# Performance work log

Hardware: AMD Instinct MI355X
Metric: run time of the kernel (lower is better)

Reference implementation:

```python
import math
import jax, jax.numpy as jnp
import numpy as np

B, S, D, H = 2, 2048, 1024, 16
DH = D // H


def setup_inputs() -> dict:
    key = jax.random.key(0)
    ks = jax.random.split(key, 12)
    s = 1.0 / math.sqrt(D)
    return {
        "x_q": jax.random.normal(ks[0], (B, S, D), jnp.float32),
        "x_k": jax.random.normal(ks[1], (B, S, D), jnp.float32),
        "x_v": jax.random.normal(ks[2], (B, S, D), jnp.float32),
        "mask": jax.random.randint(ks[3], (B, S), 0, 2) > 0,
        "Wq": jax.random.normal(ks[4], (D, D), jnp.float32) * s,
        "bq": jnp.zeros((D,), jnp.float32),
        "Wk": jax.random.normal(ks[5], (D, D), jnp.float32) * s,
        "bk": jnp.zeros((D,), jnp.float32),
        "Wv": jax.random.normal(ks[6], (D, D), jnp.float32) * s,
        "bv": jnp.zeros((D,), jnp.float32),
        "Wo": jax.random.normal(ks[7], (D, D), jnp.float32) * s,
        "bo": jnp.zeros((D,), jnp.float32),
    }


def reference(x_q, x_k, x_v, mask, Wq, bq, Wk, bk, Wv, bv, Wo, bo):
    # nn.Linear: y = x @ W^T + b
    Q = jnp.einsum('bsd,ed->bse', x_q, Wq) + bq
    K = jnp.einsum('bsd,ed->bse', x_k, Wk) + bk
    V = jnp.einsum('bsd,ed->bse', x_v, Wv) + bv
    b, sq, d = Q.shape
    # split(dim_split, 2) + cat(dim=0) == per-head attention on [B,S,H,DH]
    Qh = Q.reshape(b, sq, H, DH)
    Kh = K.reshape(b, -1, H, DH)
    Vh = V.reshape(b, -1, H, DH)
    scores = jnp.einsum('bqhd,bkhd->bhqk', Qh, Kh) / math.sqrt(DH)
    # inf_mask: -1e9 where mask is False, broadcast over heads and queries
    scores = scores + jnp.where(mask[:, None, None, :], 0.0, -1e9)
    A = jax.nn.softmax(scores, axis=-1)  # dropout is identity in eval
    out = jnp.einsum('bhqk,bkhd->bqhd', A, Vh).reshape(b, sq, d)
    return jnp.einsum('bsd,ed->bse', out, Wo) + bo
```

## Files before the change

### kernel.cpp

```cpp
#include <hip/hip_runtime.h>
#include <hip/hip_bf16.h>
#include <stdint.h>

#define BB  2
#define SS  2048
#define DDIM 1024
#define HH  16
#define DH  64

typedef __attribute__((ext_vector_type(8))) short short8;
typedef __attribute__((ext_vector_type(4))) short short4v;
typedef __attribute__((ext_vector_type(4))) float float4v;

#define AS1 __attribute__((address_space(1)))
#define AS3 __attribute__((address_space(3)))

static __device__ __forceinline__ void gl2lds16(const void* g, void* l) {
  __builtin_amdgcn_global_load_lds((const AS1 unsigned int*)g,
                                   (AS3 unsigned int*)l, 16, 0, 0);
}

static __device__ __forceinline__ float bf2f(short s) {
  union { unsigned u; float f; } c;
  c.u = ((unsigned)(unsigned short)s) << 16;
  return c.f;
}
static __device__ __forceinline__ short f2bf(float f) {
  union { float ff; unsigned u; } c;
  c.ff = f;
  unsigned u = c.u;
  u += 0x7fffu + ((u >> 16) & 1u);
  return (short)(u >> 16);
}

#if __has_builtin(__builtin_amdgcn_exp2f)
static __device__ __forceinline__ float exp2fast(float x) { return __builtin_amdgcn_exp2f(x); }
#else
static __device__ __forceinline__ float exp2fast(float x) { return __expf(x * 0.69314718056f); }
#endif

static __device__ __forceinline__ unsigned packbf(float x, float y) {
  unsigned ax = __float_as_uint(x) + 0x8000u;
  unsigned ay = __float_as_uint(y) + 0x8000u;
#if __has_builtin(__builtin_amdgcn_perm)
  return __builtin_amdgcn_perm(ay, ax, 0x07060302u);
#else
  return (ax >> 16) | (ay & 0xffff0000u);
#endif
}

static __device__ __forceinline__ int detect_f32(const void* p) {
  const float* f = (const float*)p;
  int ok = 1;
#pragma unroll
  for (int i = 0; i < 16; i++) {
    float a = fabsf(f[i]);
    ok &= (a > 1e-10f && a < 1e4f) ? 1 : 0;
  }
  return ok;
}

struct CvtArgs {
  const void* xq; const void* xk; const void* xv;
  const void* wq; const void* wk; const void* wv; const void* wo;
  const void* b0; const void* b1; const void* b2; const void* b3;
  const int* mask;
  short* dst;
  float* mw;
};

__global__ __launch_bounds__(256)
void cvt_kernel(CvtArgs a) {
  const int f32m = detect_f32(a.xq);
  const size_t gtid = (size_t)blockIdx.x * blockDim.x + threadIdx.x;
  const size_t stride = (size_t)gridDim.x * blockDim.x;
  const size_t M4 = (size_t)4 << 20, M1 = (size_t)1 << 20, TOT = (size_t)16 << 20;
  for (size_t i = gtid; i * 4 < TOT; i += stride) {
    const size_t idx = i * 4;
    const void* src;
    size_t off;
    if (idx < 3 * M4) {
      size_t xi = idx / M4;
      off = idx & (M4 - 1);
      src = (xi == 0) ? a.xq : (xi == 1) ? a.xk : a.xv;
    } else {
      size_t wi = (idx - 3 * M4) / M1;
      off = idx & (M1 - 1);
      src = (wi == 0) ? a.wq : (wi == 1) ? a.wk : (wi == 2) ? a.wv : a.wo;
    }
    short4v o;
    if (f32m) {
      float4v v = *(const float4v*)((const float*)src + off);
#pragma unroll
      for (int j = 0; j < 4; j++) o[j] = f2bf(v[j]);
    } else {
      o = *(const short4v*)((const short*)src + off);
    }
    *(short4v*)(a.dst + idx) = o;
  }
  if (gtid < 1024) {
    const void* bs[4] = {a.b0, a.b1, a.b2, a.b3};
#pragma unroll
    for (int j = 0; j < 4; j++) {
      short v = f32m ? f2bf(((const float*)bs[j])[gtid])
                     : ((const short*)bs[j])[gtid];
      a.dst[TOT + (size_t)j * 1024 + gtid] = v;
    }
  }
  if (gtid < BB * SS)
    a.mw[gtid] = a.mask[gtid] ? -23.083120654223414f : -1e9f;
}

struct GemmArgs {
  const short* x[3];
  const short* w[3];
  const short* b[3];
  short* o[3];
  const void* probe;
  int tmask;
  int detect_out;
};

__global__ __launch_bounds__(256)
void gemm_kernel(GemmArgs a) {
  constexpr int GK = 1024, GN = 1024;
  __shared__ alignas(16) short As[128 * 32];
  __shared__ alignas(16) short Bs[128 * 32];

  const int t = threadIdx.x;
  const int w = t >> 6, l = t & 63, l15 = l & 15, qd = l >> 4;
  const int bn = blockIdx.x, bm = blockIdx.y, mat = blockIdx.z;

  const short* X  = a.x[mat];
  const short* W  = a.w[mat];
  const short* Bi = a.b[mat];
  short* O        = a.o[mat];
  const int transposed = (a.tmask >> mat) & 1;

  const short* Ag = X + (size_t)bm * 128 * GK;
  const short* Bg = W + (size_t)bn * 128 * GK;

  const int L0 = t, L1 = 256 + t;
  const int r0 = L0 >> 2, g0 = (L0 & 3) ^ ((r0 >> 1) & 3);
  const int r1 = L1 >> 2, g1 = (L1 & 3) ^ ((r1 >> 1) & 3);
  const size_t off0 = (size_t)r0 * GK + g0 * 8;
  const size_t off1 = (size_t)r1 * GK + g1 * 8;

  float4v acc[4][4];
#pragma unroll
  for (int i = 0; i < 4; i++)
#pragma unroll
    for (int j = 0; j < 4; j++) acc[i][j] = (float4v){0.f, 0.f, 0.f, 0.f};

  const int wm = (w >> 1) * 64, wn = (w & 1) * 64;

  for (int k0 = 0; k0 < GK; k0 += 32) {
    gl2lds16(Ag + off0 + k0, (char*)As + L0 * 16);
    gl2lds16(Ag + off1 + k0, (char*)As + L1 * 16);
    gl2lds16(Bg + off0 + k0, (char*)Bs + L0 * 16);
    gl2lds16(Bg + off1 + k0, (char*)Bs + L1 * 16);
    __syncthreads();

    short8 af[4], bf[4];
#pragma unroll
    for (int i = 0; i < 4; i++) {
      int m = wm + i * 16 + l15;
      af[i] = *(const short8*)((const char*)As + (m * 4 + (qd ^ ((m >> 1) & 3))) * 16);
      int n = wn + i * 16 + l15;
      bf[i] = *(const short8*)((const char*)Bs + (n * 4 + (qd ^ ((n >> 1) & 3))) * 16);
    }
#pragma unroll
    for (int i = 0; i < 4; i++)
#pragma unroll
      for (int j = 0; j < 4; j++)
        acc[i][j] = __builtin_amdgcn_mfma_f32_16x16x32_bf16(af[i], bf[j], acc[i][j], 0, 0, 0);
    __syncthreads();
  }

  if (!transposed) {
    const int outf32 = a.detect_out ? detect_f32(a.probe) : 0;
    float bj[4];
#pragma unroll
    for (int j = 0; j < 4; j++) bj[j] = bf2f(Bi[bn * 128 + wn + j * 16 + l15]);
#pragma unroll
    for (int i = 0; i < 4; i++) {
      int mgl = bm * 128 + wm + i * 16 + qd * 4;
#pragma unroll
      for (int j = 0; j < 4; j++) {
        int ngl = bn * 128 + wn + j * 16 + l15;
        if (outf32) {
          float* Of = (float*)O;
#pragma unroll
          for (int r = 0; r < 4; r++)
            Of[(size_t)(mgl + r) * GN + ngl] = acc[i][j][r] + bj[j];
        } else {
#pragma unroll
          for (int r = 0; r < 4; r++)
            O[(size_t)(mgl + r) * GN + ngl] = f2bf(acc[i][j][r] + bj[j]);
        }
      }
    }
  } else {
#pragma unroll
    for (int j = 0; j < 4; j++) {
      int ngl = bn * 128 + wn + j * 16 + l15;
      float bb = bf2f(Bi[ngl]);
#pragma unroll
      for (int i = 0; i < 4; i++) {
        int mgl = bm * 128 + wm + i * 16 + qd * 4;
        int bidx = mgl >> 11;
        int s = mgl & (SS - 1);
        short4v v;
#pragma unroll
        for (int r = 0; r < 4; r++) v[r] = f2bf(acc[i][j][r] + bb);
        *(short4v*)(O + (size_t)bidx * DDIM * SS + (size_t)ngl * SS + s) = v;
      }
    }
  }
}

__global__ __launch_bounds__(128)
void flash_kernel(const short* __restrict__ Q, const short* __restrict__ K,
                  const short* __restrict__ Vt, const float* __restrict__ Mw,
                  short* __restrict__ At) {
  __shared__ alignas(16) short Kbuf[2][2][2048];
  __shared__ alignas(16) short Vbuf[2][2][2048];

  const int t = threadIdx.x;
  const int w = t >> 6, l = t & 63, l15 = l & 15, qd = l >> 4;
  const int bh = blockIdx.x, qt = blockIdx.y;
  const int b = bh >> 4, h = bh & 15;
  const int q0 = qt * 64 + w * 32;

  const float SC = 0.125f * 1.44269504f;

  short8 qf[2][2];
#pragma unroll
  for (int g = 0; g < 2; g++) {
    const short* Qb = Q + ((size_t)(b * SS + q0 + 16 * g + l15)) * DDIM + h * 64;
#pragma unroll
    for (int c = 0; c < 2; c++) qf[g][c] = *(const short8*)(Qb + 32 * c + 8 * qd);
  }

  const short ov = (l15 == 0) ? (short)0x3F80 : (short)0;
  const short8 onesf = {ov, ov, ov, ov, ov, ov, ov, ov};

  const short* Kg = K + ((size_t)(b * SS + (l >> 3))) * DDIM + h * 64
                    + ((l & 7) ^ ((l >> 3) & 7)) * 8;
  const short* Vg = Vt + (size_t)b * DDIM * SS + (size_t)(h * 64 + (l >> 2)) * SS
                    + ((l & 3) ^ ((l >> 3) & 3)) * 8;
  const float* MwB = Mw + b * SS;

  char* Kw = (char*)Kbuf[w];
  char* Vw = (char*)Vbuf[w];

  float4v oacc[2][4], oaccl[2];
#pragma unroll
  for (int g = 0; g < 2; g++) {
    oaccl[g] = (float4v){0.f, 0.f, 0.f, 0.f};
#pragma unroll
    for (int mt = 0; mt < 4; mt++) oacc[g][mt] = (float4v){0.f, 0.f, 0.f, 0.f};
  }

  const int sv2 = 2 * ((l15 >> 1) & 3);
  const int kswz = l15 & 7;

  float4v maC[2], maN[2];

  {
#pragma unroll
    for (int j = 0; j < 4; j++)
      gl2lds16(Kg + (size_t)(j * 8) * DDIM, Kw + j * 1024 + (l << 4));
#pragma unroll
    for (int j = 0; j < 4; j++)
      gl2lds16(Vg + (size_t)(j * 16) * SS, Vw + j * 1024 + (l << 4));
#pragma unroll
    for (int mt = 0; mt < 2; mt++)
      maC[mt] = *(const float4v*)(MwB + mt * 16 + 4 * qd);
  }

  auto body = [&](int i, int bb) {
    asm volatile("s_waitcnt vmcnt(0)" ::: "memory");

    if (i < 63) {
      const int nb = bb ^ 1;
      const size_t koff = (size_t)((i + 1) * 32) * DDIM;
#pragma unroll
      for (int j = 0; j < 4; j++)
        gl2lds16(Kg + koff + (size_t)(j * 8) * DDIM, Kw + nb * 4096 + j * 1024 + (l << 4));
      const int voff = (i + 1) * 32;
#pragma unroll
      for (int j = 0; j < 4; j++)
        gl2lds16(Vg + voff + (size_t)(j * 16) * SS, Vw + nb * 4096 + j * 1024 + (l << 4));
#pragma unroll
      for (int mt = 0; mt < 2; mt++)
        maN[mt] = *(const float4v*)(MwB + (i + 1) * 32 + mt * 16 + 4 * qd);
    }

    const short* ksb = (const short*)(Kw + bb * 4096);
    const short* vsb = (const short*)(Vw + bb * 4096);

    float4v sacc[2][2];
#pragma unroll
    for (int g = 0; g < 2; g++)
#pragma unroll
      for (int mt = 0; mt < 2; mt++) sacc[g][mt] = (float4v){0.f, 0.f, 0.f, 0.f};
#pragma unroll
    for (int c = 0; c < 2; c++) {
#pragma unroll
      for (int mt = 0; mt < 2; mt++) {
        short8 kf = *(const short8*)(ksb + (mt * 16 + l15) * 64 + (((c * 4 + qd) ^ kswz) * 8));
#pragma unroll
        for (int g = 0; g < 2; g++)
          sacc[g][mt] = __builtin_amdgcn_mfma_f32_16x16x32_bf16(kf, qf[g][c], sacc[g][mt], 0, 0, 0);
      }
    }

    union { short4v h[2]; short8 v8; } vf[4];
#pragma unroll
    for (int mt = 0; mt < 4; mt++) {
      const short* vr = vsb + (mt * 16 + l15) * 32;
      vf[mt].h[0] = *(const short4v*)(vr + ((qd ^ sv2) * 4));
      vf[mt].h[1] = *(const short4v*)(vr + (((4 + qd) ^ sv2) * 4));
    }

#pragma unroll
    for (int g = 0; g < 2; g++) {
      float p0[4], p1[4];
#pragma unroll
      for (int r = 0; r < 4; r++) {
        p0[r] = exp2fast(fmaf(sacc[g][0][r], SC, maC[0][r]));
        p1[r] = exp2fast(fmaf(sacc[g][1][r], SC, maC[1][r]));
      }
      union { unsigned u[4]; short8 v8; } pk;
      pk.u[0] = packbf(p0[0], p0[1]);
      pk.u[1] = packbf(p0[2], p0[3]);
      pk.u[2] = packbf(p1[0], p1[1]);
      pk.u[3] = packbf(p1[2], p1[3]);

#pragma unroll
      for (int mt = 0; mt < 4; mt++)
        oacc[g][mt] = __builtin_amdgcn_mfma_f32_16x16x32_bf16(vf[mt].v8, pk.v8, oacc[g][mt], 0, 0, 0);
      oaccl[g] = __builtin_amdgcn_mfma_f32_16x16x32_bf16(onesf, pk.v8, oaccl[g], 0, 0, 0);
    }

    maC[0] = maN[0];
    maC[1] = maN[1];
  };

  for (int i = 0; i < 64; i += 2) {
    body(i, 0);
    body(i + 1, 1);
  }

#pragma unroll
  for (int g = 0; g < 2; g++) {
    const float lg = __shfl(oaccl[g][0], l15);
    const float inv = 1.f / lg;
    short* Og = At + ((size_t)(b * SS + q0 + 16 * g + l15)) * DDIM + h * 64;
#pragma unroll
    for (int mt = 0; mt < 4; mt++) {
      short4v v;
#pragma unroll
      for (int r = 0; r < 4; r++) v[r] = f2bf(oacc[g][mt][r] * inv);
      *(short4v*)(Og + mt * 16 + qd * 4) = v;
    }
  }
}

extern "C" void kernel_launch(void* const* d_in, const int* in_sizes, int n_in,
                              void* d_out, int out_size, void* d_ws, size_t ws_size,
                              hipStream_t stream) {
  (void)in_sizes; (void)n_in; (void)out_size; (void)ws_size;
  const int* mask = (const int*)d_in[3];

  char* ws = (char*)d_ws;
  short* wsBF = (short*)ws;
  const size_t M1 = (size_t)1 << 20;
  short* Qb = (short*)(ws + (size_t)34 * M1);
  short* Kb = (short*)(ws + (size_t)42 * M1);
  short* Vt = (short*)(ws + (size_t)50 * M1);
  short* At = (short*)(ws + (size_t)58 * M1);
  float* Mw = (float*)(ws + (size_t)66 * M1);

  CvtArgs c;
  c.xq = d_in[0]; c.xk = d_in[1]; c.xv = d_in[2];
  c.wq = d_in[4]; c.wk = d_in[6]; c.wv = d_in[8]; c.wo = d_in[10];
  c.b0 = d_in[5]; c.b1 = d_in[7]; c.b2 = d_in[9]; c.b3 = d_in[11];
  c.mask = mask; c.dst = wsBF; c.mw = Mw;
  hipLaunchKernelGGL(cvt_kernel, dim3(4096), dim3(256), 0, stream, c);

  GemmArgs a1;
  a1.x[0] = wsBF;            a1.x[1] = wsBF + 4 * M1;  a1.x[2] = wsBF + 8 * M1;
  a1.w[0] = wsBF + 12 * M1;  a1.w[1] = wsBF + 13 * M1; a1.w[2] = wsBF + 14 * M1;
  a1.b[0] = wsBF + 16 * M1;  a1.b[1] = wsBF + 16 * M1 + 1024;
  a1.b[2] = wsBF + 16 * M1 + 2048;
  a1.o[0] = Qb; a1.o[1] = Kb; a1.o[2] = Vt;
  a1.probe = d_in[0];
  a1.tmask = 4;
  a1.detect_out = 0;
  hipLaunchKernelGGL(gemm_kernel, dim3(8, 32, 3), dim3(256), 0, stream, a1);

  hipLaunchKernelGGL(flash_kernel, dim3(32, 32), dim3(128), 0, stream,
                     Qb, Kb, Vt, Mw, At);

  GemmArgs a2;
  a2.x[0] = At;             a2.w[0] = wsBF + 15 * M1;
  a2.b[0] = wsBF + 16 * M1 + 3072;
  a2.o[0] = (short*)d_out;
  a2.x[1] = a2.x[2] = At; a2.w[1] = a2.w[2] = a2.w[0];
  a2.b[1] = a2.b[2] = a2.b[0]; a2.o[1] = a2.o[2] = a2.o[0];
  a2.probe = d_in[0];
  a2.tmask = 0;
  a2.detect_out = 1;
  hipLaunchKernelGGL(gemm_kernel, dim3(8, 32, 1), dim3(256), 0, stream, a2);
}
```

Measured before the change: 263.4 us.

## Load K/V tiles directly into registers and use single-wave flash blocks

The flash attention kernel drops the LDS staging of K and V tiles. Each lane now loads its MFMA operand fragments straight from global memory into double-buffered register sets, and the software pipeline alternates between A and B tiles. The launch becomes one 64-thread wave per block, with batch-head as the fastest-varying index so that blocks sharing K/V run together and hit in L2. This removes the LDS round trip and the waitcnt stalls, at the cost of less coalesced global loads and higher register pressure.

Result: slower. 375.7 us (+42.6%).

```diff
diff --git a/kernel.cpp b/kernel.cpp
--- a/kernel.cpp
+++ b/kernel.cpp
@@ -219,18 +219,15 @@
   }
 }
 
-__global__ __launch_bounds__(128)
+__global__ __launch_bounds__(64)
 void flash_kernel(const short* __restrict__ Q, const short* __restrict__ K,
                   const short* __restrict__ Vt, const float* __restrict__ Mw,
                   short* __restrict__ At) {
-  __shared__ alignas(16) short Kbuf[2][2][2048];
-  __shared__ alignas(16) short Vbuf[2][2][2048];
-
-  const int t = threadIdx.x;
-  const int w = t >> 6, l = t & 63, l15 = l & 15, qd = l >> 4;
-  const int bh = blockIdx.x, qt = blockIdx.y;
+  const int l = threadIdx.x, l15 = l & 15, qd = l >> 4;
+  const int x = blockIdx.x;
+  const int bh = x & 31, qt = x >> 5;
   const int b = bh >> 4, h = bh & 15;
-  const int q0 = qt * 64 + w * 32;
+  const int q0 = qt * 32;
 
   const float SC = 0.125f * 1.44269504f;
 
@@ -245,14 +242,20 @@
   const short ov = (l15 == 0) ? (short)0x3F80 : (short)0;
   const short8 onesf = {ov, ov, ov, ov, ov, ov, ov, ov};
 
-  const short* Kg = K + ((size_t)(b * SS + (l >> 3))) * DDIM + h * 64
-                    + ((l & 7) ^ ((l >> 3) & 7)) * 8;
-  const short* Vg = Vt + (size_t)b * DDIM * SS + (size_t)(h * 64 + (l >> 2)) * SS
-                    + ((l & 3) ^ ((l >> 3) & 3)) * 8;
-  const float* MwB = Mw + b * SS;
-
-  char* Kw = (char*)Kbuf[w];
-  char* Vw = (char*)Vbuf[w];
+  const short* kp[2];
+#pragma unroll
+  for (int mt = 0; mt < 2; mt++)
+    kp[mt] = K + ((size_t)(b * SS + 16 * mt + l15)) * DDIM + h * 64 + 8 * qd;
+  const short* vp[4];
+#pragma unroll
+  for (int mt = 0; mt < 4; mt++)
+    vp[mt] = Vt + (size_t)b * DDIM * SS + (size_t)(h * 64 + 16 * mt + l15) * SS + 4 * qd;
+  const float* mp = Mw + b * SS + 4 * qd;
+
+  short8 kfA[2][2], kfB[2][2];
+  union VF { short4v h[2]; short8 v8; };
+  VF vfA[4], vfB[4];
+  float4v maA[2], maB[2];
 
   float4v oacc[2][4], oaccl[2];
 #pragma unroll
@@ -262,96 +265,63 @@
     for (int mt = 0; mt < 4; mt++) oacc[g][mt] = (float4v){0.f, 0.f, 0.f, 0.f};
   }
 
-  const int sv2 = 2 * ((l15 >> 1) & 3);
-  const int kswz = l15 & 7;
-
-  float4v maC[2], maN[2];
-
-  {
-#pragma unroll
-    for (int j = 0; j < 4; j++)
-      gl2lds16(Kg + (size_t)(j * 8) * DDIM, Kw + j * 1024 + (l << 4));
-#pragma unroll
-    for (int j = 0; j < 4; j++)
-      gl2lds16(Vg + (size_t)(j * 16) * SS, Vw + j * 1024 + (l << 4));
-#pragma unroll
-    for (int mt = 0; mt < 2; mt++)
-      maC[mt] = *(const float4v*)(MwB + mt * 16 + 4 * qd);
-  }
-
-  auto body = [&](int i, int bb) {
-    asm volatile("s_waitcnt vmcnt(0)" ::: "memory");
-
-    if (i < 63) {
-      const int nb = bb ^ 1;
-      const size_t koff = (size_t)((i + 1) * 32) * DDIM;
-#pragma unroll
-      for (int j = 0; j < 4; j++)
-        gl2lds16(Kg + koff + (size_t)(j * 8) * DDIM, Kw + nb * 4096 + j * 1024 + (l << 4));
-      const int voff = (i + 1) * 32;
-#pragma unroll
-      for (int j = 0; j < 4; j++)
-        gl2lds16(Vg + voff + (size_t)(j * 16) * SS, Vw + nb * 4096 + j * 1024 + (l << 4));
+#define LOAD_TILE(KF, VF_, MA, i)                                              \
+  do {                                                                         \
+    const size_t krow = (size_t)(i) * 32 * DDIM;                               \
+    _Pragma("unroll") for (int mt = 0; mt < 2; mt++) {                         \
+      KF[mt][0] = *(const short8*)(kp[mt] + krow);                             \
+      KF[mt][1] = *(const short8*)(kp[mt] + krow + 32);                        \
+    }                                                                          \
+    _Pragma("unroll") for (int mt = 0; mt < 4; mt++) {                         \
+      VF_[mt].h[0] = *(const short4v*)(vp[mt] + (i) * 32);                     \
+      VF_[mt].h[1] = *(const short4v*)(vp[mt] + (i) * 32 + 16);                \
+    }                                                                          \
+    _Pragma("unroll") for (int mt = 0; mt < 2; mt++)                           \
+      MA[mt] = *(const float4v*)(mp + (i) * 32 + 16 * mt);                     \
+  } while (0)
+
+  auto compute = [&](short8 kf[2][2], VF vf[4], float4v ma[2]) {
+    float4v sacc[2][2];
+#pragma unroll
+    for (int g = 0; g < 2; g++)
+#pragma unroll
+      for (int mt = 0; mt < 2; mt++) sacc[g][mt] = (float4v){0.f, 0.f, 0.f, 0.f};
+#pragma unroll
+    for (int c = 0; c < 2; c++)
 #pragma unroll
       for (int mt = 0; mt < 2; mt++)
-        maN[mt] = *(const float4v*)(MwB + (i + 1) * 32 + mt * 16 + 4 * qd);
-    }
-
-    const short* ksb = (const short*)(Kw + bb * 4096);
-    const short* vsb = (const short*)(Vw + bb * 4096);
-
-    float4v sacc[2][2];
-#pragma unroll
-    for (int g = 0; g < 2; g++)
-#pragma unroll
-      for (int mt = 0; mt < 2; mt++) sacc[g][mt] = (float4v){0.f, 0.f, 0.f, 0.f};
-#pragma unroll
-    for (int c = 0; c < 2; c++) {
-#pragma unroll
-      for (int mt = 0; mt < 2; mt++) {
-        short8 kf = *(const short8*)(ksb + (mt * 16 + l15) * 64 + (((c * 4 + qd) ^ kswz) * 8));
 #pragma unroll
         for (int g = 0; g < 2; g++)
-          sacc[g][mt] = __builtin_amdgcn_mfma_f32_16x16x32_bf16(kf, qf[g][c], sacc[g][mt], 0, 0, 0);
-      }
-    }
-
-    union { short4v h[2]; short8 v8; } vf[4];
-#pragma unroll
-    for (int mt = 0; mt < 4; mt++) {
-      const short* vr = vsb + (mt * 16 + l15) * 32;
-      vf[mt].h[0] = *(const short4v*)(vr + ((qd ^ sv2) * 4));
-      vf[mt].h[1] = *(const short4v*)(vr + (((4 + qd) ^ sv2) * 4));
-    }
+          sacc[g][mt] = __builtin_amdgcn_mfma_f32_16x16x32_bf16(kf[mt][c], qf[g][c], sacc[g][mt], 0, 0, 0);
 
 #pragma unroll
     for (int g = 0; g < 2; g++) {
       float p0[4], p1[4];
 #pragma unroll
       for (int r = 0; r < 4; r++) {
-        p0[r] = exp2fast(fmaf(sacc[g][0][r], SC, maC[0][r]));
-        p1[r] = exp2fast(fmaf(sacc[g][1][r], SC, maC[1][r]));
+        p0[r] = exp2fast(fmaf(sacc[g][0][r], SC, ma[0][r]));
+        p1[r] = exp2fast(fmaf(sacc[g][1][r], SC, ma[1][r]));
       }
       union { unsigned u[4]; short8 v8; } pk;
       pk.u[0] = packbf(p0[0], p0[1]);
       pk.u[1] = packbf(p0[2], p0[3]);
       pk.u[2] = packbf(p1[0], p1[1]);
       pk.u[3] = packbf(p1[2], p1[3]);
-
 #pragma unroll
       for (int mt = 0; mt < 4; mt++)
         oacc[g][mt] = __builtin_amdgcn_mfma_f32_16x16x32_bf16(vf[mt].v8, pk.v8, oacc[g][mt], 0, 0, 0);
       oaccl[g] = __builtin_amdgcn_mfma_f32_16x16x32_bf16(onesf, pk.v8, oaccl[g], 0, 0, 0);
     }
-
-    maC[0] = maN[0];
-    maC[1] = maN[1];
   };
 
+  LOAD_TILE(kfA, vfA, maA, 0);
   for (int i = 0; i < 64; i += 2) {
-    body(i, 0);
-    body(i + 1, 1);
-  }
+    if (i + 1 < 64) LOAD_TILE(kfB, vfB, maB, i + 1);
+    compute(kfA, vfA, maA);
+    if (i + 2 < 64) LOAD_TILE(kfA, vfA, maA, i + 2);
+    compute(kfB, vfB, maB);
+  }
+#undef LOAD_TILE
 
 #pragma unroll
   for (int g = 0; g < 2; g++) {
@@ -401,7 +371,7 @@
   a1.detect_out = 0;
   hipLaunchKernelGGL(gemm_kernel, dim3(8, 32, 3), dim3(256), 0, stream, a1);
 
-  hipLaunchKernelGGL(flash_kernel, dim3(32, 32), dim3(128), 0, stream,
+  hipLaunchKernelGGL(flash_kernel, dim3(64 * 32), dim3(64), 0, stream,
                      Qb, Kb, Vt, Mw, At);
 
   GemmArgs a2;
```

## Share K/V tiles across four waves in flash attention with block barriers

Applied to the files above, without the earlier changes.

The flash kernel moves from 2-wave blocks, where each wave loads its own 32-key K/V slices, to 4-wave blocks covering 128 queries. The four waves now share double-buffered 64-key K and V tiles in LDS, loaded cooperatively, plus a small mask-add buffer. This cuts redundant global-to-LDS traffic per query and halves the iteration count. In exchange it adds a block-wide barrier every iteration, halves the grid size, and changes the LDS swizzle for V.

New measurement: 245.9 us. 6.6% less time.

```diff
diff --git a/kernel.cpp b/kernel.cpp
--- a/kernel.cpp
+++ b/kernel.cpp
@@ -219,18 +219,19 @@
   }
 }
 
-__global__ __launch_bounds__(128)
+__global__ __launch_bounds__(256)
 void flash_kernel(const short* __restrict__ Q, const short* __restrict__ K,
                   const short* __restrict__ Vt, const float* __restrict__ Mw,
                   short* __restrict__ At) {
-  __shared__ alignas(16) short Kbuf[2][2][2048];
-  __shared__ alignas(16) short Vbuf[2][2][2048];
+  __shared__ alignas(16) short Ks[2][64 * 64];
+  __shared__ alignas(16) short Vs[2][64 * 64];
+  __shared__ alignas(16) float madd[2][64];
 
   const int t = threadIdx.x;
   const int w = t >> 6, l = t & 63, l15 = l & 15, qd = l >> 4;
   const int bh = blockIdx.x, qt = blockIdx.y;
   const int b = bh >> 4, h = bh & 15;
-  const int q0 = qt * 64 + w * 32;
+  const int q0 = qt * 128 + w * 32;
 
   const float SC = 0.125f * 1.44269504f;
 
@@ -245,14 +246,13 @@
   const short ov = (l15 == 0) ? (short)0x3F80 : (short)0;
   const short8 onesf = {ov, ov, ov, ov, ov, ov, ov, ov};
 
-  const short* Kg = K + ((size_t)(b * SS + (l >> 3))) * DDIM + h * 64
-                    + ((l & 7) ^ ((l >> 3) & 7)) * 8;
-  const short* Vg = Vt + (size_t)b * DDIM * SS + (size_t)(h * 64 + (l >> 2)) * SS
-                    + ((l & 3) ^ ((l >> 3) & 3)) * 8;
+  const int kr = t >> 3;
+  const short* Kg = K + ((size_t)(b * SS + kr)) * DDIM + h * 64
+                    + ((t & 7) ^ (kr & 7)) * 8;
+  const int vr = t >> 3;
+  const short* Vg = Vt + (size_t)b * DDIM * SS + (size_t)(h * 64 + vr) * SS
+                    + ((t & 7) ^ (vr & 7)) * 8;
   const float* MwB = Mw + b * SS;
-
-  char* Kw = (char*)Kbuf[w];
-  char* Vw = (char*)Vbuf[w];
 
   float4v oacc[2][4], oaccl[2];
 #pragma unroll
@@ -262,95 +262,90 @@
     for (int mt = 0; mt < 4; mt++) oacc[g][mt] = (float4v){0.f, 0.f, 0.f, 0.f};
   }
 
-  const int sv2 = 2 * ((l15 >> 1) & 3);
-  const int kswz = l15 & 7;
-
-  float4v maC[2], maN[2];
-
-  {
-#pragma unroll
-    for (int j = 0; j < 4; j++)
-      gl2lds16(Kg + (size_t)(j * 8) * DDIM, Kw + j * 1024 + (l << 4));
-#pragma unroll
-    for (int j = 0; j < 4; j++)
-      gl2lds16(Vg + (size_t)(j * 16) * SS, Vw + j * 1024 + (l << 4));
-#pragma unroll
-    for (int mt = 0; mt < 2; mt++)
-      maC[mt] = *(const float4v*)(MwB + mt * 16 + 4 * qd);
-  }
-
-  auto body = [&](int i, int bb) {
-    asm volatile("s_waitcnt vmcnt(0)" ::: "memory");
-
-    if (i < 63) {
-      const int nb = bb ^ 1;
-      const size_t koff = (size_t)((i + 1) * 32) * DDIM;
-#pragma unroll
-      for (int j = 0; j < 4; j++)
-        gl2lds16(Kg + koff + (size_t)(j * 8) * DDIM, Kw + nb * 4096 + j * 1024 + (l << 4));
-      const int voff = (i + 1) * 32;
-#pragma unroll
-      for (int j = 0; j < 4; j++)
-        gl2lds16(Vg + voff + (size_t)(j * 16) * SS, Vw + nb * 4096 + j * 1024 + (l << 4));
-#pragma unroll
-      for (int mt = 0; mt < 2; mt++)
-        maN[mt] = *(const float4v*)(MwB + (i + 1) * 32 + mt * 16 + 4 * qd);
-    }
-
-    const short* ksb = (const short*)(Kw + bb * 4096);
-    const short* vsb = (const short*)(Vw + bb * 4096);
-
-    float4v sacc[2][2];
+  const int swz = l15 & 7;
+
+  gl2lds16(Kg, (char*)Ks[0] + t * 16);
+  gl2lds16(Kg + (size_t)32 * DDIM, (char*)Ks[0] + 4096 + t * 16);
+  gl2lds16(Vg, (char*)Vs[0] + t * 16);
+  gl2lds16(Vg + 32 * SS, (char*)Vs[0] + 4096 + t * 16);
+  float mwN = 0.f;
+  if (t < 64) {
+    madd[0][t] = MwB[t];
+    mwN = MwB[64 + t];
+  }
+
+  for (int i = 0; i < 32; i++) {
+    const int cur = i & 1, nxt = cur ^ 1;
+    asm volatile("s_waitcnt vmcnt(0) lgkmcnt(0)\n\ts_barrier" ::: "memory");
+
+    if (i < 31) {
+      const size_t ko = (size_t)((i + 1) * 64) * DDIM;
+      gl2lds16(Kg + ko, (char*)Ks[nxt] + t * 16);
+      gl2lds16(Kg + ko + (size_t)32 * DDIM, (char*)Ks[nxt] + 4096 + t * 16);
+      const int vo = (i + 1) * 64;
+      gl2lds16(Vg + vo, (char*)Vs[nxt] + t * 16);
+      gl2lds16(Vg + vo + 32 * SS, (char*)Vs[nxt] + 4096 + t * 16);
+    }
+    if (t < 64) {
+      madd[nxt][t] = mwN;
+      int idx = (i + 2) * 64 + t;
+      if (idx > SS - 1) idx = SS - 1;
+      mwN = MwB[idx];
+    }
+
+    const short* ksb = Ks[cur];
+    const short* vsb = Vs[cur];
+
+    float4v sacc[2][4];
 #pragma unroll
     for (int g = 0; g < 2; g++)
 #pragma unroll
-      for (int mt = 0; mt < 2; mt++) sacc[g][mt] = (float4v){0.f, 0.f, 0.f, 0.f};
-#pragma unroll
-    for (int c = 0; c < 2; c++) {
-#pragma unroll
-      for (int mt = 0; mt < 2; mt++) {
-        short8 kf = *(const short8*)(ksb + (mt * 16 + l15) * 64 + (((c * 4 + qd) ^ kswz) * 8));
+      for (int mt = 0; mt < 4; mt++) sacc[g][mt] = (float4v){0.f, 0.f, 0.f, 0.f};
+#pragma unroll
+    for (int mt = 0; mt < 4; mt++) {
+#pragma unroll
+      for (int c = 0; c < 2; c++) {
+        short8 kf = *(const short8*)(ksb + (mt * 16 + l15) * 64 + (((4 * c + qd) ^ swz) * 8));
 #pragma unroll
         for (int g = 0; g < 2; g++)
           sacc[g][mt] = __builtin_amdgcn_mfma_f32_16x16x32_bf16(kf, qf[g][c], sacc[g][mt], 0, 0, 0);
       }
     }
 
-    union { short4v h[2]; short8 v8; } vf[4];
-#pragma unroll
-    for (int mt = 0; mt < 4; mt++) {
-      const short* vr = vsb + (mt * 16 + l15) * 32;
-      vf[mt].h[0] = *(const short4v*)(vr + ((qd ^ sv2) * 4));
-      vf[mt].h[1] = *(const short4v*)(vr + (((4 + qd) ^ sv2) * 4));
-    }
-
-#pragma unroll
-    for (int g = 0; g < 2; g++) {
-      float p0[4], p1[4];
-#pragma unroll
-      for (int r = 0; r < 4; r++) {
-        p0[r] = exp2fast(fmaf(sacc[g][0][r], SC, maC[0][r]));
-        p1[r] = exp2fast(fmaf(sacc[g][1][r], SC, maC[1][r]));
+    float4v ma[4];
+#pragma unroll
+    for (int mt = 0; mt < 4; mt++)
+      ma[mt] = *(const float4v*)(&madd[cur][16 * mt + 4 * qd]);
+
+#pragma unroll
+    for (int pp = 0; pp < 2; pp++) {
+      union { short4v h[2]; short8 v8; } vf[4];
+#pragma unroll
+      for (int mt = 0; mt < 4; mt++) {
+        const short* vrp = vsb + (mt * 16 + l15) * 64;
+        const int u0 = 8 * pp + qd, u1 = 8 * pp + 4 + qd;
+        vf[mt].h[0] = *(const short4v*)(vrp + (((u0 >> 1) ^ swz) * 8) + (u0 & 1) * 4);
+        vf[mt].h[1] = *(const short4v*)(vrp + (((u1 >> 1) ^ swz) * 8) + (u1 & 1) * 4);
       }
-      union { unsigned u[4]; short8 v8; } pk;
-      pk.u[0] = packbf(p0[0], p0[1]);
-      pk.u[1] = packbf(p0[2], p0[3]);
-      pk.u[2] = packbf(p1[0], p1[1]);
-      pk.u[3] = packbf(p1[2], p1[3]);
-
-#pragma unroll
-      for (int mt = 0; mt < 4; mt++)
-        oacc[g][mt] = __builtin_amdgcn_mfma_f32_16x16x32_bf16(vf[mt].v8, pk.v8, oacc[g][mt], 0, 0, 0);
-      oaccl[g] = __builtin_amdgcn_mfma_f32_16x16x32_bf16(onesf, pk.v8, oaccl[g], 0, 0, 0);
-    }
-
-    maC[0] = maN[0];
-    maC[1] = maN[1];
-  };
-
-  for (int i = 0; i < 64; i += 2) {
-    body(i, 0);
-    body(i + 1, 1);
+#pragma unroll
+      for (int g = 0; g < 2; g++) {
+        float p0[4], p1[4];
+#pragma unroll
+        for (int r = 0; r < 4; r++) {
+          p0[r] = exp2fast(fmaf(sacc[g][2 * pp][r],     SC, ma[2 * pp][r]));
+          p1[r] = exp2fast(fmaf(sacc[g][2 * pp + 1][r], SC, ma[2 * pp + 1][r]));
+        }
+        union { unsigned u[4]; short8 v8; } pk;
+        pk.u[0] = packbf(p0[0], p0[1]);
+        pk.u[1] = packbf(p0[2], p0[3]);
+        pk.u[2] = packbf(p1[0], p1[1]);
+        pk.u[3] = packbf(p1[2], p1[3]);
+#pragma unroll
+        for (int mt = 0; mt < 4; mt++)
+          oacc[g][mt] = __builtin_amdgcn_mfma_f32_16x16x32_bf16(vf[mt].v8, pk.v8, oacc[g][mt], 0, 0, 0);
+        oaccl[g] = __builtin_amdgcn_mfma_f32_16x16x32_bf16(onesf, pk.v8, oaccl[g], 0, 0, 0);
+      }
+    }
   }
 
 #pragma unroll
@@ -401,7 +396,7 @@
   a1.detect_out = 0;
   hipLaunchKernelGGL(gemm_kernel, dim3(8, 32, 3), dim3(256), 0, stream, a1);
 
-  hipLaunchKernelGGL(flash_kernel, dim3(32, 32), dim3(128), 0, stream,
+  hipLaunchKernelGGL(flash_kernel, dim3(32, 16), dim3(256), 0, stream,
                      Qb, Kb, Vt, Mw, At);
 
   GemmArgs a2;
```
